# Kernel tuning notes

Measured on AMD Instinct MI355X. Metric: run time of the kernel, lower is better.

## Reference

```python
import jax, jax.numpy as jnp
import numpy as np

N, C_IN, C_H, C_OUT, E, L = 100000, 64, 128, 16, 1600000, 3
LN_EPS = 1e-5


def setup_inputs() -> dict:
    key = jax.random.key(0)
    ks = jax.random.split(key, 16)
    d = {}
    d["x"] = jax.random.normal(ks[0], (N, C_IN), jnp.float32)
    d["edge_index_1"] = jax.random.randint(ks[1], (2, E), 0, N, jnp.int32)
    d["edge_index_2"] = jax.random.randint(ks[2], (2, E), 0, N, jnp.int32)

    def lin(k, fi, fo):
        s = 1.0 / np.sqrt(fi)
        return jax.random.uniform(k, (fi, fo), jnp.float32, -s, s)

    d["enc_w"] = lin(ks[3], C_IN, C_H)
    d["enc_b"] = jnp.zeros((C_H,), jnp.float32)
    for l in range(L):
        d[f"conv_w{l}"] = lin(ks[4 + l], C_H, C_H)
        d[f"conv_b{l}"] = jnp.zeros((C_H,), jnp.float32)
        d[f"ln_g{l}"] = jnp.ones((C_H,), jnp.float32)
        d[f"ln_b{l}"] = jnp.zeros((C_H,), jnp.float32)
    d["out_w"] = lin(ks[10], 2 * C_H, C_OUT)
    d["out_b"] = jnp.zeros((C_OUT,), jnp.float32)
    return d


def layer_norm(x, g, b):
    m = jnp.mean(x, axis=-1, keepdims=True)
    v = jnp.mean(jnp.square(x - m), axis=-1, keepdims=True)
    return (x - m) * jax.lax.rsqrt(v + LN_EPS) * g + b


def gcn_conv(x, src, dst, w, b):
    # PyG GCNConv: add self-loops, symmetric normalization, then aggregate.
    h = x @ w  # [N, C_H]
    deg = jax.ops.segment_sum(jnp.ones(src.shape[0], h.dtype), dst, num_segments=N) + 1.0
    dis = jax.lax.rsqrt(deg)  # deg^{-1/2}, deg >= 1 so finite
    msg = h[src] * (dis[src] * dis[dst])[:, None]  # [E, C_H] gather + scale
    agg = jax.ops.segment_sum(msg, dst, num_segments=N)
    agg = agg + h * (dis * dis)[:, None]  # self-loop term
    return agg + b


def _branch(x, src, dst, p):
    # feature encoder (Linear + ReLU; dropout is identity at eval)
    x = jax.nn.relu(x @ p["enc_w"] + p["enc_b"])
    for l in range(L):
        x = gcn_conv(x, src, dst, p[f"conv_w{l}"], p[f"conv_b{l}"])
        x = jax.nn.relu(layer_norm(x, p[f"ln_g{l}"], p[f"ln_b{l}"]))
    return x


def reference(x, edge_index_1, edge_index_2, enc_w, enc_b,
              conv_w0, conv_b0, ln_g0, ln_b0,
              conv_w1, conv_b1, ln_g1, ln_b1,
              conv_w2, conv_b2, ln_g2, ln_b2,
              out_w, out_b):
    p = dict(enc_w=enc_w, enc_b=enc_b,
             conv_w0=conv_w0, conv_b0=conv_b0, ln_g0=ln_g0, ln_b0=ln_b0,
             conv_w1=conv_w1, conv_b1=conv_b1, ln_g1=ln_g1, ln_b1=ln_b1,
             conv_w2=conv_w2, conv_b2=conv_b2, ln_g2=ln_g2, ln_b2=ln_b2)
    # layers_1 and layers_2 share the same underlying modules -> shared weights
    x1 = _branch(x, edge_index_1[0], edge_index_1[1], p)
    x2 = _branch(x, edge_index_2[0], edge_index_2[1], p)
    fused = jnp.concatenate([x1, x2], axis=-1)  # middle_layer == 'concat'
    return fused @ out_w + out_b
```

## Files before the change

### kernel.cpp

```cpp
#include <hip/hip_runtime.h>

#define NN 100000
#define LN_EPS 1e-5f
#define BSH 6
#define BNODES 64
#define NBK ((NN + 63) >> 6)
#define EC 6144

typedef unsigned int uint_t;
typedef unsigned short ushort_t;
typedef __attribute__((ext_vector_type(8))) short short8v;
typedef __attribute__((ext_vector_type(4))) float f32x4;


__device__ __forceinline__ uint_t cvtpk(float a, float b) {
  uint_t ua = __float_as_uint(a);
  ua = (ua + 0x7FFFu + ((ua >> 16) & 1u)) >> 16;
  uint_t ub = __float_as_uint(b);
  ub = (ub + 0x7FFFu + ((ub >> 16) & 1u)) & 0xFFFF0000u;
  return ua | ub;
}
__device__ __forceinline__ ushort_t bf16_1(float x) {
  uint_t u = __float_as_uint(x);
  return (ushort_t)((u + 0x7FFFu + ((u >> 16) & 1u)) >> 16);
}
__device__ __forceinline__ float bf_lo(uint_t u) { return __uint_as_float(u << 16); }
__device__ __forceinline__ float bf_hi(uint_t u) { return __uint_as_float(u & 0xFFFF0000u); }


__global__ __launch_bounds__(256) void k_scanA32(const int* in0, const int* in1,
                                                 int* out0, int* out1,
                                                 int* bsum0, int* bsum1, int n) {
  const int* in = blockIdx.y ? in1 : in0;
  int* out = blockIdx.y ? out1 : out0;
  int* bsum = blockIdx.y ? bsum1 : bsum0;
  __shared__ int sh[256];
  int t = threadIdx.x;
  int base = blockIdx.x * 8192 + t * 32;
  int v[32];
  int s = 0;
#pragma unroll
  for (int i = 0; i < 32; ++i) {
    int idx = base + i;
    v[i] = (idx < n) ? in[idx] : 0;
    s += v[i];
  }
  sh[t] = s;
  __syncthreads();
  for (int d = 1; d < 256; d <<= 1) {
    int a = (t >= d) ? sh[t - d] : 0;
    __syncthreads();
    sh[t] += a;
    __syncthreads();
  }
  int run = sh[t] - s;
  if (t == 255) bsum[blockIdx.x] = sh[255];
#pragma unroll
  for (int i = 0; i < 32; ++i) {
    int idx = base + i;
    if (idx < n) out[idx] = run;
    run += v[i];
  }
}

__global__ void k_scanB(int* bsum0, int* bsum1, int nb) {
  int* bsum = blockIdx.y ? bsum1 : bsum0;
  int t = threadIdx.x;
  int x = (t < nb) ? bsum[t] : 0;
  int incl = x;
#pragma unroll
  for (int d = 1; d < 64; d <<= 1) {
    int y = __shfl_up(incl, d, 64);
    if (t >= d) incl += y;
  }
  if (t < nb) bsum[t] = incl - x;
}

__global__ void k_scanC32(int* rp0, int* rp1, const int* bsum0, const int* bsum1,
                          int n, int total) {
  int* rp = blockIdx.y ? rp1 : rp0;
  const int* bsum = blockIdx.y ? bsum1 : bsum0;
  int i = blockIdx.x * 256 + threadIdx.x;
  if (i < n) rp[i] += bsum[i >> 13];
  else if (i == n) rp[n] = total;
}


__global__ __launch_bounds__(256) void k_phist(const int* dst0, const int* dst1,
                                               int* gmatC0, int* gmatC1, int E, int B) {
  const int* dst = blockIdx.y ? dst1 : dst0;
  int* gmatC = blockIdx.y ? gmatC1 : gmatC0;
  __shared__ int lh[NBK];
  int t = threadIdx.x;
  for (int i = t; i < NBK; i += 256) lh[i] = 0;
  __syncthreads();
  int base = blockIdx.x * EC;
  int end = min(E, base + EC);
  for (int i = base + t; i < end; i += 256) atomicAdd(&lh[dst[i] >> BSH], 1);
  __syncthreads();
  for (int b = t; b < NBK; b += 256) gmatC[(size_t)b * B + blockIdx.x] = lh[b];
}

__global__ __launch_bounds__(256) void k_pscatter(const int* src0, const int* src1,
                                                  const int* dst0, const int* dst1,
                                                  const int* gmatS0, const int* gmatS1,
                                                  uint_t* parts0, uint_t* parts1,
                                                  int E, int B) {
  const int* src = blockIdx.y ? src1 : src0;
  const int* dst = blockIdx.y ? dst1 : dst0;
  const int* gmatS = blockIdx.y ? gmatS1 : gmatS0;
  uint_t* parts = blockIdx.y ? parts1 : parts0;
  __shared__ uint_t stage[EC];
  __shared__ int lh[2048];
  __shared__ int lcur[NBK];
  __shared__ int sh[256];
  int t = threadIdx.x;
  int c = blockIdx.x;
  for (int i = t; i < 2048; i += 256) lh[i] = 0;
  __syncthreads();
  int base = c * EC;
  int end = min(E, base + EC);
  int cnt = end - base;
  for (int i = base + t; i < end; i += 256) atomicAdd(&lh[dst[i] >> BSH], 1);
  __syncthreads();
  int loc[8];
  int s = 0;
#pragma unroll
  for (int i = 0; i < 8; ++i) {
    loc[i] = lh[t * 8 + i];
    s += loc[i];
  }
  sh[t] = s;
  __syncthreads();
  for (int d = 1; d < 256; d <<= 1) {
    int a = (t >= d) ? sh[t - d] : 0;
    __syncthreads();
    sh[t] += a;
    __syncthreads();
  }
  int run = sh[t] - s;
#pragma unroll
  for (int i = 0; i < 8; ++i) {
    int v = loc[i];
    lh[t * 8 + i] = run;
    run += v;
  }
  __syncthreads();
  for (int i = t; i < NBK; i += 256) lcur[i] = lh[i];
  __syncthreads();
  for (int i = base + t; i < end; i += 256) {
    int d = dst[i];
    int b = d >> BSH;
    int pos = atomicAdd(&lcur[b], 1);
    stage[pos] = ((uint_t)(d & (BNODES - 1)) << 20) | (uint_t)src[i];
  }
  __syncthreads();
  for (int i = t; i < cnt; i += 256) {
    int lo = 0, hi = NBK;
    while (hi - lo > 1) {
      int mid = (lo + hi) >> 1;
      if (lh[mid] <= i) lo = mid; else hi = mid;
    }
    int gb = gmatS[(size_t)lo * B + c];
    parts[gb + (i - lh[lo])] = stage[i];
  }
}


__global__ __launch_bounds__(256) void k_degb2(const uint_t* parts0, const uint_t* parts1,
                                               const int* gmatS0, const int* gmatS1,
                                               int* absRp0, int* absRp1,
                                               int* csrc0, int* csrc1,
                                               float* dis0, float* dis1, int B, int n) {
  const uint_t* parts = blockIdx.y ? parts1 : parts0;
  const int* gmatS = blockIdx.y ? gmatS1 : gmatS0;
  int* absRp = blockIdx.y ? absRp1 : absRp0;
  int* csrc = blockIdx.y ? csrc1 : csrc0;
  float* dis = blockIdx.y ? dis1 : dis0;
  __shared__ int cnt[BNODES];
  __shared__ int lcur[BNODES];
  __shared__ int sEx[BNODES + 1];
  int t = threadIdx.x;
  int b = blockIdx.x;
  if (t < BNODES) cnt[t] = 0;
  __syncthreads();
  int s0 = gmatS[(size_t)b * B];
  int s1 = gmatS[(size_t)(b + 1) * B];
  for (int i = s0 + t; i < s1; i += 256) atomicAdd(&cnt[parts[i] >> 20], 1);
  __syncthreads();
  if (t < BNODES) {
    int c = cnt[t];
    int incl = c;
#pragma unroll
    for (int d = 1; d < 64; d <<= 1) {
      int y = __shfl_up(incl, d, 64);
      if (t >= d) incl += y;
    }
    sEx[t] = s0 + incl - c;
    lcur[t] = s0 + incl - c;
    if (t == 63) sEx[64] = s0 + incl;
    int node = (b << BSH) + t;
    if (node < n) dis[node] = rsqrtf((float)(c + 1));
  }
  __syncthreads();
  if (t < BNODES + 1) absRp[(size_t)b * 65 + t] = sEx[t];
  for (int i = s0 + t; i < s1; i += 256) {
    uint_t u = parts[i];
    int dl = u >> 20;
    int pos = atomicAdd(&lcur[dl], 1);
    csrc[pos] = (int)((u & 0xFFFFFu) << 8);
  }
}


__global__ void k_prep(const float* W0, const float* W1, const float* W2,
                       const float* W3, ushort_t* P0, ushort_t* P1,
                       ushort_t* P2, ushort_t* P3,
                       const float* __restrict__ x, ushort_t* __restrict__ xb,
                       int total4) {
  int y = blockIdx.y;
  if (y < 4) {
    const float* W = (y == 0) ? W0 : (y == 1) ? W1 : (y == 2) ? W2 : W3;
    ushort_t* P = (y == 0) ? P0 : (y == 1) ? P1 : (y == 2) ? P2 : P3;
    int lim = (y == 3) ? 1024 : 2048;
    int t = blockIdx.x * 256 + threadIdx.x;
    if (t >= lim) return;
    int lane = t & 63;
    int j = (t >> 6) & 7;
    int kk = t >> 9;
    int krow = kk * 32 + (lane >> 4) * 8;
    int col = j * 16 + (lane & 15);
    uint4 v;
    v.x = cvtpk(W[(size_t)(krow + 0) * 128 + col], W[(size_t)(krow + 1) * 128 + col]);
    v.y = cvtpk(W[(size_t)(krow + 2) * 128 + col], W[(size_t)(krow + 3) * 128 + col]);
    v.z = cvtpk(W[(size_t)(krow + 4) * 128 + col], W[(size_t)(krow + 5) * 128 + col]);
    v.w = cvtpk(W[(size_t)(krow + 6) * 128 + col], W[(size_t)(krow + 7) * 128 + col]);
    *(uint4*)&P[(size_t)t * 8] = v;
  } else {
    int i = blockIdx.x * 256 + threadIdx.x;
    if (i < total4) {
      float4 v = *(const float4*)&x[i * 4];
      uint2 p;
      p.x = cvtpk(v.x, v.y);
      p.y = cvtpk(v.z, v.w);
      *(uint2*)&xb[i * 4] = p;
    }
  }
}


template <int KK>
__global__ __launch_bounds__(256) void k_gemm_enc(const ushort_t* __restrict__ A,
                                                  const ushort_t* __restrict__ Wp,
                                                  const float* __restrict__ bias,
                                                  ushort_t* __restrict__ C, int n) {
  int lane = threadIdx.x & 63;
  int wid = threadIdx.x >> 6;
  int r0 = (blockIdx.x * 4 + wid) * 16;
  if (r0 >= n) return;
  int arow = r0 + (lane & 15);
  if (arow >= n) arow = n - 1;
  const ushort_t* aptr = A + (size_t)arow * (KK * 32) + (lane >> 4) * 8;

  f32x4 acc[8] = {};
#pragma unroll
  for (int kk = 0; kk < KK; ++kk) {
    short8v a = *(const short8v*)(aptr + kk * 32);
    const ushort_t* wp = Wp + ((size_t)(kk * 8) * 64 + lane) * 8;
#pragma unroll
    for (int j = 0; j < 8; ++j) {
      short8v b = *(const short8v*)(wp + (size_t)j * 512);
      acc[j] = __builtin_amdgcn_mfma_f32_16x16x32_bf16(a, b, acc[j], 0, 0, 0);
    }
  }
  int rbase = r0 + (lane >> 4) * 4;
  int colb = lane & 15;
  float bcol[8];
#pragma unroll
  for (int j = 0; j < 8; ++j) bcol[j] = bias[j * 16 + colb];
#pragma unroll
  for (int reg = 0; reg < 4; ++reg) {
    int row = rbase + reg;
    if (row < n) {
#pragma unroll
      for (int j = 0; j < 8; ++j)
        C[(size_t)row * 128 + j * 16 + colb] = bf16_1(fmaxf(acc[j][reg] + bcol[j], 0.f));
    }
  }
}

__global__ __launch_bounds__(256) void k_gemm_mfma2(const ushort_t* __restrict__ A,
                                                    const ushort_t* __restrict__ Wp,
                                                    const float* __restrict__ dis1,
                                                    const float* __restrict__ dis2,
                                                    ushort_t* __restrict__ C1,
                                                    ushort_t* __restrict__ C2, int n) {
  int lane = threadIdx.x & 63;
  int wid = threadIdx.x >> 6;
  int r0 = (blockIdx.x * 4 + wid) * 16;
  if (r0 >= n) return;
  int arow = r0 + (lane & 15);
  if (arow >= n) arow = n - 1;
  const ushort_t* aptr = A + (size_t)arow * 128 + (lane >> 4) * 8;

  f32x4 acc[8] = {};
#pragma unroll
  for (int kk = 0; kk < 4; ++kk) {
    short8v a = *(const short8v*)(aptr + kk * 32);
    const ushort_t* wp = Wp + ((size_t)(kk * 8) * 64 + lane) * 8;
#pragma unroll
    for (int j = 0; j < 8; ++j) {
      short8v b = *(const short8v*)(wp + (size_t)j * 512);
      acc[j] = __builtin_amdgcn_mfma_f32_16x16x32_bf16(a, b, acc[j], 0, 0, 0);
    }
  }
  int rbase = r0 + (lane >> 4) * 4;
  int colb = lane & 15;
#pragma unroll
  for (int reg = 0; reg < 4; ++reg) {
    int row = rbase + reg;
    if (row < n) {
      float s1 = dis1[row];
      float s2 = dis2[row];
#pragma unroll
      for (int j = 0; j < 8; ++j) {
        float v = acc[j][reg];
        C1[(size_t)row * 128 + j * 16 + colb] = bf16_1(v * s1);
        C2[(size_t)row * 128 + j * 16 + colb] = bf16_1(v * s2);
      }
    }
  }
}

__global__ __launch_bounds__(256) void k_gemm_dual(const ushort_t* A0, const ushort_t* A1,
                                                   const ushort_t* __restrict__ Wp,
                                                   const float* dis0, const float* dis1,
                                                   ushort_t* C0, ushort_t* C1, int n) {
  int br = blockIdx.y;
  const ushort_t* A = br ? A1 : A0;
  const float* dis = br ? dis1 : dis0;
  ushort_t* C = br ? C1 : C0;
  int lane = threadIdx.x & 63;
  int wid = threadIdx.x >> 6;
  int r0 = (blockIdx.x * 4 + wid) * 16;
  if (r0 >= n) return;
  int arow = r0 + (lane & 15);
  if (arow >= n) arow = n - 1;
  const ushort_t* aptr = A + (size_t)arow * 128 + (lane >> 4) * 8;

  f32x4 acc[8] = {};
#pragma unroll
  for (int kk = 0; kk < 4; ++kk) {
    short8v a = *(const short8v*)(aptr + kk * 32);
    const ushort_t* wp = Wp + ((size_t)(kk * 8) * 64 + lane) * 8;
#pragma unroll
    for (int j = 0; j < 8; ++j) {
      short8v b = *(const short8v*)(wp + (size_t)j * 512);
      acc[j] = __builtin_amdgcn_mfma_f32_16x16x32_bf16(a, b, acc[j], 0, 0, 0);
    }
  }
  int rbase = r0 + (lane >> 4) * 4;
  int colb = lane & 15;
#pragma unroll
  for (int reg = 0; reg < 4; ++reg) {
    int row = rbase + reg;
    if (row < n) {
      float s = dis[row];
#pragma unroll
      for (int j = 0; j < 8; ++j)
        C[(size_t)row * 128 + j * 16 + colb] = bf16_1(acc[j][reg] * s);
    }
  }
}


#define ACC8(U)                                                   \
  a0 += bf_lo(U.x); a1 += bf_hi(U.x); a2 += bf_lo(U.y); a3 += bf_hi(U.y); \
  a4 += bf_lo(U.z); a5 += bf_hi(U.z); a6 += bf_lo(U.w); a7 += bf_hi(U.w);

__global__ __launch_bounds__(256) void k_agg_dual(const char* hwb0, const char* hwb1,
                                                  const int* rpA, const int* rpB,
                                                  const int* csrc0, const int* csrc1,
                                                  const float* dis0, const float* dis1,
                                                  const float* __restrict__ bias,
                                                  const float* __restrict__ g,
                                                  const float* __restrict__ bln,
                                                  uint4* out0, uint4* out1, int n) {
  int br = blockIdx.y;
  const char* hwb = br ? hwb1 : hwb0;
  const int* rp = br ? rpB : rpA;
  const int* csrc = br ? csrc1 : csrc0;
  const float* dis = br ? dis1 : dis0;
  uint4* out4 = br ? out1 : out0;

  __shared__ int sidx[4][64];
  int lane = threadIdx.x & 63;
  int wv = threadIdx.x >> 6;
  int q = lane >> 4;
  int cl = lane & 15;
  int clOff = cl << 4;
  int node = blockIdx.x * 4 + wv;
  if (node >= n) return;
  int ridx = node + (node >> 6);
  int start = rp[ridx];
  int endAbs = rp[ridx + 1];
  float a0 = 0.f, a1 = 0.f, a2 = 0.f, a3 = 0.f, a4 = 0.f, a5 = 0.f, a6 = 0.f, a7 = 0.f;

  int base = start;
  while (base < endAbs) {
    int take = min(endAbs - base, 64);
    if (lane < take) sidx[wv][lane] = csrc[base + lane];
    int e = q;
    for (; e + 12 < take; e += 16) {
      int o0 = sidx[wv][e] + clOff;
      int o1 = sidx[wv][e + 4] + clOff;
      int o2 = sidx[wv][e + 8] + clOff;
      int o3 = sidx[wv][e + 12] + clOff;
      uint4 u = *(const uint4*)(hwb + o0);
      uint4 v = *(const uint4*)(hwb + o1);
      uint4 w = *(const uint4*)(hwb + o2);
      uint4 z = *(const uint4*)(hwb + o3);
      ACC8(u); ACC8(v); ACC8(w); ACC8(z);
    }
    for (; e < take; e += 4) {
      int o0 = sidx[wv][e] + clOff;
      uint4 u = *(const uint4*)(hwb + o0);
      ACC8(u);
    }
    base += take;
  }
#pragma unroll
  for (int m = 16; m < 64; m <<= 1) {
    a0 += __shfl_xor(a0, m, 64); a1 += __shfl_xor(a1, m, 64);
    a2 += __shfl_xor(a2, m, 64); a3 += __shfl_xor(a3, m, 64);
    a4 += __shfl_xor(a4, m, 64); a5 += __shfl_xor(a5, m, 64);
    a6 += __shfl_xor(a6, m, 64); a7 += __shfl_xor(a7, m, 64);
  }
  uint4 us = *(const uint4*)(hwb + node * 256 + clOff);
  ACC8(us);
  float dn = dis[node];
  float4 b0 = *(const float4*)&bias[cl * 8];
  float4 b1 = *(const float4*)&bias[cl * 8 + 4];
  a0 = fmaf(a0, dn, b0.x); a1 = fmaf(a1, dn, b0.y);
  a2 = fmaf(a2, dn, b0.z); a3 = fmaf(a3, dn, b0.w);
  a4 = fmaf(a4, dn, b1.x); a5 = fmaf(a5, dn, b1.y);
  a6 = fmaf(a6, dn, b1.z); a7 = fmaf(a7, dn, b1.w);
  float s1v = a0 + a1 + a2 + a3 + a4 + a5 + a6 + a7;
  float s2v = a0 * a0 + a1 * a1 + a2 * a2 + a3 * a3 +
              a4 * a4 + a5 * a5 + a6 * a6 + a7 * a7;
#pragma unroll
  for (int m = 1; m < 16; m <<= 1) {
    s1v += __shfl_xor(s1v, m, 64);
    s2v += __shfl_xor(s2v, m, 64);
  }
  float mean = s1v * (1.0f / 128.0f);
  float var = s2v * (1.0f / 128.0f) - mean * mean;
  float rstd = rsqrtf(var + LN_EPS);
  float4 g0 = *(const float4*)&g[cl * 8];
  float4 g1 = *(const float4*)&g[cl * 8 + 4];
  float4 l0 = *(const float4*)&bln[cl * 8];
  float4 l1 = *(const float4*)&bln[cl * 8 + 4];
  float y0 = fmaxf(fmaf((a0 - mean) * rstd, g0.x, l0.x), 0.f);
  float y1 = fmaxf(fmaf((a1 - mean) * rstd, g0.y, l0.y), 0.f);
  float y2 = fmaxf(fmaf((a2 - mean) * rstd, g0.z, l0.z), 0.f);
  float y3 = fmaxf(fmaf((a3 - mean) * rstd, g0.w, l0.w), 0.f);
  float y4 = fmaxf(fmaf((a4 - mean) * rstd, g1.x, l1.x), 0.f);
  float y5 = fmaxf(fmaf((a5 - mean) * rstd, g1.y, l1.y), 0.f);
  float y6 = fmaxf(fmaf((a6 - mean) * rstd, g1.z, l1.z), 0.f);
  float y7 = fmaxf(fmaf((a7 - mean) * rstd, g1.w, l1.w), 0.f);
  if (q == 0) {
    uint4 p;
    p.x = cvtpk(y0, y1);
    p.y = cvtpk(y2, y3);
    p.z = cvtpk(y4, y5);
    p.w = cvtpk(y6, y7);
    out4[(size_t)node * 16 + cl] = p;
  }
}


__global__ __launch_bounds__(256) void k_out(const ushort_t* __restrict__ x1,
                                             const ushort_t* __restrict__ x2,
                                             const float* __restrict__ w,
                                             const float* __restrict__ b,
                                             float* __restrict__ out, int n) {
  __shared__ float wl[256 * 16];
  __shared__ float bl[16];
  int tid = threadIdx.x;
#pragma unroll
  for (int i = 0; i < 4; ++i) {
    int idx = (i * 256 + tid) * 4;
    *(float4*)&wl[idx] = *(const float4*)&w[idx];
  }
  if (tid < 16) bl[tid] = b[tid];
  __syncthreads();
  int node = blockIdx.x * 256 + tid;
  if (node >= n) return;
  float acc[16];
#pragma unroll
  for (int o = 0; o < 16; ++o) acc[o] = bl[o];

  const ushort_t* xr = x1 + (size_t)node * 128;
#pragma unroll 2
  for (int c = 0; c < 128; c += 8) {
    uint4 xv = *(const uint4*)&xr[c];
    float f0 = bf_lo(xv.x), f1 = bf_hi(xv.x), f2 = bf_lo(xv.y), f3 = bf_hi(xv.y);
    float f4 = bf_lo(xv.z), f5 = bf_hi(xv.z), f6 = bf_lo(xv.w), f7 = bf_hi(xv.w);
#pragma unroll
    for (int o = 0; o < 16; ++o) {
      acc[o] = fmaf(f0, wl[(c + 0) * 16 + o],
               fmaf(f1, wl[(c + 1) * 16 + o],
               fmaf(f2, wl[(c + 2) * 16 + o],
               fmaf(f3, wl[(c + 3) * 16 + o],
               fmaf(f4, wl[(c + 4) * 16 + o],
               fmaf(f5, wl[(c + 5) * 16 + o],
               fmaf(f6, wl[(c + 6) * 16 + o],
               fmaf(f7, wl[(c + 7) * 16 + o], acc[o]))))))));
    }
  }
  const ushort_t* xr2 = x2 + (size_t)node * 128;
#pragma unroll 2
  for (int c = 0; c < 128; c += 8) {
    uint4 xv = *(const uint4*)&xr2[c];
    float f0 = bf_lo(xv.x), f1 = bf_hi(xv.x), f2 = bf_lo(xv.y), f3 = bf_hi(xv.y);
    float f4 = bf_lo(xv.z), f5 = bf_hi(xv.z), f6 = bf_lo(xv.w), f7 = bf_hi(xv.w);
#pragma unroll
    for (int o = 0; o < 16; ++o) {
      acc[o] = fmaf(f0, wl[(128 + c + 0) * 16 + o],
               fmaf(f1, wl[(128 + c + 1) * 16 + o],
               fmaf(f2, wl[(128 + c + 2) * 16 + o],
               fmaf(f3, wl[(128 + c + 3) * 16 + o],
               fmaf(f4, wl[(128 + c + 4) * 16 + o],
               fmaf(f5, wl[(128 + c + 5) * 16 + o],
               fmaf(f6, wl[(128 + c + 6) * 16 + o],
               fmaf(f7, wl[(128 + c + 7) * 16 + o], acc[o]))))))));
    }
  }
#pragma unroll
  for (int o = 0; o < 4; ++o) {
    *(float4*)&out[(size_t)node * 16 + o * 4] =
        make_float4(acc[o * 4], acc[o * 4 + 1], acc[o * 4 + 2], acc[o * 4 + 3]);
  }
}


extern "C" void kernel_launch(void* const* d_in, const int* in_sizes, int n_in,
                              void* d_out, int out_size, void* d_ws, size_t ws_size,
                              hipStream_t stream) {
  const float* x = (const float*)d_in[0];
  const int* ei1 = (const int*)d_in[1];
  const int* ei2 = (const int*)d_in[2];
  const float* enc_w = (const float*)d_in[3];
  const float* enc_b = (const float*)d_in[4];
  const float* conv_w[3] = {(const float*)d_in[5], (const float*)d_in[9], (const float*)d_in[13]};
  const float* conv_b[3] = {(const float*)d_in[6], (const float*)d_in[10], (const float*)d_in[14]};
  const float* ln_g[3] = {(const float*)d_in[7], (const float*)d_in[11], (const float*)d_in[15]};
  const float* ln_b[3] = {(const float*)d_in[8], (const float*)d_in[12], (const float*)d_in[16]};
  const float* out_w = (const float*)d_in[17];
  const float* out_b = (const float*)d_in[18];
  float* out = (float*)d_out;

  const int N = NN;
  const int E = in_sizes[1] / 2;
  const int B = (E + EC - 1) / EC;
  const int M = NBK * B;

  char* ws = (char*)d_ws;
  size_t off = 0;
  auto alloc = [&](size_t bytes) -> char* {
    char* p = ws + off;
    off += (bytes + 255) & ~(size_t)255;
    return p;
  };
  ushort_t* h0 = (ushort_t*)alloc((size_t)N * 128 * 2);
  ushort_t* hb = (ushort_t*)alloc((size_t)N * 128 * 2);
  ushort_t* hb2 = (ushort_t*)alloc((size_t)N * 128 * 2);
  ushort_t* p1 = (ushort_t*)alloc((size_t)N * 128 * 2);
  ushort_t* p2 = (ushort_t*)alloc((size_t)N * 128 * 2);
  ushort_t* xb = (ushort_t*)alloc((size_t)N * 64 * 2);
  ushort_t* wpk[3];
  for (int l = 0; l < 3; ++l) wpk[l] = (ushort_t*)alloc(2048 * 8 * 2);
  ushort_t* wpe = (ushort_t*)alloc(1024 * 8 * 2);

  struct G {
    float* dis; int* absRp; int* gmatC; int* gmatS; int* bsum;
    uint_t* parts; int* csrc; const int* src; const int* dst;
  } g[2];
  for (int i = 0; i < 2; ++i) {
    g[i].dis = (float*)alloc((size_t)N * 4);
    g[i].absRp = (int*)alloc((size_t)NBK * 65 * 4);
    g[i].gmatC = (int*)alloc((size_t)M * 4);
    g[i].gmatS = (int*)alloc((size_t)(M + 1) * 4);
    g[i].bsum = (int*)alloc(64 * 4);
    g[i].parts = (uint_t*)alloc((size_t)E * 4);
    g[i].csrc = (int*)alloc((size_t)(E + 64) * 4);
  }
  g[0].src = ei1; g[0].dst = ei1 + E;
  g[1].src = ei2; g[1].dst = ei2 + E;

  int nScanM = (M + 8191) / 8192;

  k_phist<<<dim3(B, 2), 256, 0, stream>>>(g[0].dst, g[1].dst, g[0].gmatC, g[1].gmatC, E, B);
  k_scanA32<<<dim3(nScanM, 2), 256, 0, stream>>>(g[0].gmatC, g[1].gmatC,
                                                 g[0].gmatS, g[1].gmatS,
                                                 g[0].bsum, g[1].bsum, M);
  k_scanB<<<dim3(1, 2), 64, 0, stream>>>(g[0].bsum, g[1].bsum, nScanM);
  k_scanC32<<<dim3((M + 1 + 255) / 256, 2), 256, 0, stream>>>(g[0].gmatS, g[1].gmatS,
                                                              g[0].bsum, g[1].bsum, M, E);
  k_pscatter<<<dim3(B, 2), 256, 0, stream>>>(g[0].src, g[1].src, g[0].dst, g[1].dst,
                                             g[0].gmatS, g[1].gmatS,
                                             g[0].parts, g[1].parts, E, B);
  k_degb2<<<dim3(NBK, 2), 256, 0, stream>>>(g[0].parts, g[1].parts,
                                            g[0].gmatS, g[1].gmatS,
                                            g[0].absRp, g[1].absRp,
                                            g[0].csrc, g[1].csrc,
                                            g[0].dis, g[1].dis, B, N);

  int total4 = N * 64 / 4;
  k_prep<<<dim3((total4 + 255) / 256, 5), 256, 0, stream>>>(
      conv_w[0], conv_w[1], conv_w[2], enc_w, wpk[0], wpk[1], wpk[2], wpe,
      x, xb, total4);

  int gb = (N + 63) / 64;
  int ga = (N + 3) / 4;
  k_gemm_enc<2><<<gb, 256, 0, stream>>>(xb, wpe, enc_b, h0, N);

  k_gemm_mfma2<<<gb, 256, 0, stream>>>(h0, wpk[0], g[0].dis, g[1].dis, hb, hb2, N);
  k_agg_dual<<<dim3(ga, 2), 256, 0, stream>>>((const char*)hb, (const char*)hb2,
                                              g[0].absRp, g[1].absRp,
                                              g[0].csrc, g[1].csrc,
                                              g[0].dis, g[1].dis,
                                              conv_b[0], ln_g[0], ln_b[0],
                                              (uint4*)p1, (uint4*)p2, N);
  for (int l = 1; l < 3; ++l) {
    k_gemm_dual<<<dim3(gb, 2), 256, 0, stream>>>(p1, p2, wpk[l], g[0].dis, g[1].dis,
                                                 hb, hb2, N);
    k_agg_dual<<<dim3(ga, 2), 256, 0, stream>>>((const char*)hb, (const char*)hb2,
                                                g[0].absRp, g[1].absRp,
                                                g[0].csrc, g[1].csrc,
                                                g[0].dis, g[1].dis,
                                                conv_b[l], ln_g[l], ln_b[l],
                                                (uint4*)p1, (uint4*)p2, N);
  }

  k_out<<<(N + 255) / 256, 256, 0, stream>>>(p1, p2, out_w, out_b, out, N);
}
```

Before: 608.5 us.

## Fuse encoder and layer-0 GEMMs via LDS, cache dst indices, hoist agg loads

The encoder GEMM and the first conv GEMM now run in one kernel. The encoder output tile goes into LDS and feeds the second MFMA GEMM directly, so the intermediate h0 buffer is no longer written to and read back from global memory. The partition-scatter kernel keeps the dst indices it read in the first pass in a per-thread array and reuses them in the second pass instead of reloading them. The aggregation kernel issues its self-term, bias and LayerNorm parameter loads before the edge loop so their latency overlaps the gather. The register array is indexed dynamically and may spill to scratch memory.

```diff
diff --git a/kernel.cpp b/kernel.cpp
--- a/kernel.cpp
+++ b/kernel.cpp
@@ -121,7 +121,13 @@
   int base = c * EC;
   int end = min(E, base + EC);
   int cnt = end - base;
-  for (int i = base + t; i < end; i += 256) atomicAdd(&lh[dst[i] >> BSH], 1);
+  int dreg[EC / 256];
+  int nIt = 0;
+  for (int i = base + t; i < end; i += 256) {
+    int d = dst[i];
+    dreg[nIt++] = d;
+    atomicAdd(&lh[d >> BSH], 1);
+  }
   __syncthreads();
   int loc[8];
   int s = 0;
@@ -148,8 +154,9 @@
   __syncthreads();
   for (int i = t; i < NBK; i += 256) lcur[i] = lh[i];
   __syncthreads();
+  nIt = 0;
   for (int i = base + t; i < end; i += 256) {
-    int d = dst[i];
+    int d = dreg[nIt++];
     int b = d >> BSH;
     int pos = atomicAdd(&lcur[b], 1);
     stage[pos] = ((uint_t)(d & (BNODES - 1)) << 20) | (uint_t)src[i];
@@ -249,84 +256,75 @@
 }
 
 
-template <int KK>
-__global__ __launch_bounds__(256) void k_gemm_enc(const ushort_t* __restrict__ A,
-                                                  const ushort_t* __restrict__ Wp,
-                                                  const float* __restrict__ bias,
-                                                  ushort_t* __restrict__ C, int n) {
+__global__ __launch_bounds__(256) void k_enc_l0(const ushort_t* __restrict__ A,
+                                                const ushort_t* __restrict__ Wpe,
+                                                const float* __restrict__ bias,
+                                                const ushort_t* __restrict__ Wp0,
+                                                const float* __restrict__ dis1,
+                                                const float* __restrict__ dis2,
+                                                ushort_t* __restrict__ C1,
+                                                ushort_t* __restrict__ C2, int n) {
+  __shared__ ushort_t tile[4][16][136];
   int lane = threadIdx.x & 63;
-  int wid = threadIdx.x >> 6;
-  int r0 = (blockIdx.x * 4 + wid) * 16;
+  int wv = threadIdx.x >> 6;
+  int r0 = (blockIdx.x * 4 + wv) * 16;
   if (r0 >= n) return;
   int arow = r0 + (lane & 15);
   if (arow >= n) arow = n - 1;
-  const ushort_t* aptr = A + (size_t)arow * (KK * 32) + (lane >> 4) * 8;
-
-  f32x4 acc[8] = {};
-#pragma unroll
-  for (int kk = 0; kk < KK; ++kk) {
-    short8v a = *(const short8v*)(aptr + kk * 32);
-    const ushort_t* wp = Wp + ((size_t)(kk * 8) * 64 + lane) * 8;
-#pragma unroll
-    for (int j = 0; j < 8; ++j) {
-      short8v b = *(const short8v*)(wp + (size_t)j * 512);
-      acc[j] = __builtin_amdgcn_mfma_f32_16x16x32_bf16(a, b, acc[j], 0, 0, 0);
-    }
-  }
-  int rbase = r0 + (lane >> 4) * 4;
   int colb = lane & 15;
-  float bcol[8];
-#pragma unroll
-  for (int j = 0; j < 8; ++j) bcol[j] = bias[j * 16 + colb];
-#pragma unroll
-  for (int reg = 0; reg < 4; ++reg) {
-    int row = rbase + reg;
-    if (row < n) {
+
+  {
+    const ushort_t* aptr = A + (size_t)arow * 64 + (lane >> 4) * 8;
+    f32x4 acc[8] = {};
+#pragma unroll
+    for (int kk = 0; kk < 2; ++kk) {
+      short8v a = *(const short8v*)(aptr + kk * 32);
+      const ushort_t* wp = Wpe + ((size_t)(kk * 8) * 64 + lane) * 8;
+#pragma unroll
+      for (int j = 0; j < 8; ++j) {
+        short8v b = *(const short8v*)(wp + (size_t)j * 512);
+        acc[j] = __builtin_amdgcn_mfma_f32_16x16x32_bf16(a, b, acc[j], 0, 0, 0);
+      }
+    }
+    int rb = (lane >> 4) * 4;
+    float bcol[8];
+#pragma unroll
+    for (int j = 0; j < 8; ++j) bcol[j] = bias[j * 16 + colb];
+#pragma unroll
+    for (int reg = 0; reg < 4; ++reg) {
 #pragma unroll
       for (int j = 0; j < 8; ++j)
-        C[(size_t)row * 128 + j * 16 + colb] = bf16_1(fmaxf(acc[j][reg] + bcol[j], 0.f));
-    }
-  }
-}
-
-__global__ __launch_bounds__(256) void k_gemm_mfma2(const ushort_t* __restrict__ A,
-                                                    const ushort_t* __restrict__ Wp,
-                                                    const float* __restrict__ dis1,
-                                                    const float* __restrict__ dis2,
-                                                    ushort_t* __restrict__ C1,
-                                                    ushort_t* __restrict__ C2, int n) {
-  int lane = threadIdx.x & 63;
-  int wid = threadIdx.x >> 6;
-  int r0 = (blockIdx.x * 4 + wid) * 16;
-  if (r0 >= n) return;
-  int arow = r0 + (lane & 15);
-  if (arow >= n) arow = n - 1;
-  const ushort_t* aptr = A + (size_t)arow * 128 + (lane >> 4) * 8;
-
-  f32x4 acc[8] = {};
-#pragma unroll
-  for (int kk = 0; kk < 4; ++kk) {
-    short8v a = *(const short8v*)(aptr + kk * 32);
-    const ushort_t* wp = Wp + ((size_t)(kk * 8) * 64 + lane) * 8;
-#pragma unroll
-    for (int j = 0; j < 8; ++j) {
-      short8v b = *(const short8v*)(wp + (size_t)j * 512);
-      acc[j] = __builtin_amdgcn_mfma_f32_16x16x32_bf16(a, b, acc[j], 0, 0, 0);
-    }
-  }
-  int rbase = r0 + (lane >> 4) * 4;
-  int colb = lane & 15;
-#pragma unroll
-  for (int reg = 0; reg < 4; ++reg) {
-    int row = rbase + reg;
-    if (row < n) {
-      float s1 = dis1[row];
-      float s2 = dis2[row];
+        tile[wv][rb + reg][j * 16 + colb] = bf16_1(fmaxf(acc[j][reg] + bcol[j], 0.f));
+    }
+  }
+  __syncthreads();
+
+  {
+    const ushort_t* aptr = &tile[wv][lane & 15][(lane >> 4) * 8];
+    f32x4 acc[8] = {};
+#pragma unroll
+    for (int kk = 0; kk < 4; ++kk) {
+      short8v a = *(const short8v*)(aptr + kk * 32);
+      const ushort_t* wp = Wp0 + ((size_t)(kk * 8) * 64 + lane) * 8;
 #pragma unroll
       for (int j = 0; j < 8; ++j) {
-        float v = acc[j][reg];
-        C1[(size_t)row * 128 + j * 16 + colb] = bf16_1(v * s1);
-        C2[(size_t)row * 128 + j * 16 + colb] = bf16_1(v * s2);
+        short8v b = *(const short8v*)(wp + (size_t)j * 512);
+        acc[j] = __builtin_amdgcn_mfma_f32_16x16x32_bf16(a, b, acc[j], 0, 0, 0);
+      }
+    }
+    int rbase = r0 + (lane >> 4) * 4;
+#pragma unroll
+    for (int reg = 0; reg < 4; ++reg) {
+      int row = rbase + reg;
+      if (row < n) {
+        float s1 = dis1[row];
+        float s2 = dis2[row];
+#pragma unroll
+        for (int j = 0; j < 8; ++j) {
+          float v = acc[j][reg];
+          C1[(size_t)row * 128 + j * 16 + colb] = bf16_1(v * s1);
+          C2[(size_t)row * 128 + j * 16 + colb] = bf16_1(v * s2);
+        }
       }
     }
   }
@@ -404,6 +402,16 @@
   int ridx = node + (node >> 6);
   int start = rp[ridx];
   int endAbs = rp[ridx + 1];
+
+  uint4 us = *(const uint4*)(hwb + node * 256 + clOff);
+  float dn = dis[node];
+  float4 b0 = *(const float4*)&bias[cl * 8];
+  float4 b1 = *(const float4*)&bias[cl * 8 + 4];
+  float4 g0 = *(const float4*)&g[cl * 8];
+  float4 g1 = *(const float4*)&g[cl * 8 + 4];
+  float4 l0 = *(const float4*)&bln[cl * 8];
+  float4 l1 = *(const float4*)&bln[cl * 8 + 4];
+
   float a0 = 0.f, a1 = 0.f, a2 = 0.f, a3 = 0.f, a4 = 0.f, a5 = 0.f, a6 = 0.f, a7 = 0.f;
 
   int base = start;
@@ -436,11 +444,7 @@
     a4 += __shfl_xor(a4, m, 64); a5 += __shfl_xor(a5, m, 64);
     a6 += __shfl_xor(a6, m, 64); a7 += __shfl_xor(a7, m, 64);
   }
-  uint4 us = *(const uint4*)(hwb + node * 256 + clOff);
   ACC8(us);
-  float dn = dis[node];
-  float4 b0 = *(const float4*)&bias[cl * 8];
-  float4 b1 = *(const float4*)&bias[cl * 8 + 4];
   a0 = fmaf(a0, dn, b0.x); a1 = fmaf(a1, dn, b0.y);
   a2 = fmaf(a2, dn, b0.z); a3 = fmaf(a3, dn, b0.w);
   a4 = fmaf(a4, dn, b1.x); a5 = fmaf(a5, dn, b1.y);
@@ -456,10 +460,6 @@
   float mean = s1v * (1.0f / 128.0f);
   float var = s2v * (1.0f / 128.0f) - mean * mean;
   float rstd = rsqrtf(var + LN_EPS);
-  float4 g0 = *(const float4*)&g[cl * 8];
-  float4 g1 = *(const float4*)&g[cl * 8 + 4];
-  float4 l0 = *(const float4*)&bln[cl * 8];
-  float4 l1 = *(const float4*)&bln[cl * 8 + 4];
   float y0 = fmaxf(fmaf((a0 - mean) * rstd, g0.x, l0.x), 0.f);
   float y1 = fmaxf(fmaf((a1 - mean) * rstd, g0.y, l0.y), 0.f);
   float y2 = fmaxf(fmaf((a2 - mean) * rstd, g0.z, l0.z), 0.f);
@@ -572,7 +572,6 @@
     off += (bytes + 255) & ~(size_t)255;
     return p;
   };
-  ushort_t* h0 = (ushort_t*)alloc((size_t)N * 128 * 2);
   ushort_t* hb = (ushort_t*)alloc((size_t)N * 128 * 2);
   ushort_t* hb2 = (ushort_t*)alloc((size_t)N * 128 * 2);
   ushort_t* p1 = (ushort_t*)alloc((size_t)N * 128 * 2);
@@ -623,9 +622,9 @@
 
   int gb = (N + 63) / 64;
   int ga = (N + 3) / 4;
-  k_gemm_enc<2><<<gb, 256, 0, stream>>>(xb, wpe, enc_b, h0, N);
-
-  k_gemm_mfma2<<<gb, 256, 0, stream>>>(h0, wpk[0], g[0].dis, g[1].dis, hb, hb2, N);
+
+  k_enc_l0<<<gb, 256, 0, stream>>>(xb, wpe, enc_b, wpk[0], g[0].dis, g[1].dis,
+                                   hb, hb2, N);
   k_agg_dual<<<dim3(ga, 2), 256, 0, stream>>>((const char*)hb, (const char*)hb2,
                                               g[0].absRp, g[1].absRp,
                                               g[0].csrc, g[1].csrc,
```

Measured after the change: 653.1 us. 7.3% more time.
